# Performance work log

Measured on AMD Instinct MI355X. Metric: run time of the kernel, lower is better.

## Reference

```python
import jax, jax.numpy as jnp
import numpy as np

B, T, H = 64, 1024, 256

def _lstm_cell(x, h, c, Wih, Whh, bih, bhh):
    # torch gate order: i, f, g, o
    gates = x @ Wih.T + h @ Whh.T + bih + bhh  # [B, 4H]
    i, f, g, o = jnp.split(gates, 4, axis=-1)
    i = jax.nn.sigmoid(i)
    f = jax.nn.sigmoid(f)
    g = jnp.tanh(g)
    o = jax.nn.sigmoid(o)
    c_new = f * c + i * g
    h_new = o * jnp.tanh(c_new)
    return h_new, c_new


def setup_inputs() -> dict:
    key = jax.random.key(0)
    ks = jax.random.split(key, 11)
    s = 1.0 / np.sqrt(H)
    def u(k, shape):
        return jax.random.uniform(k, shape, jnp.float32, -s, s)
    return {
        "x": jax.random.normal(ks[0], (B, T, 1), jnp.float32),
        "enc_Wih": u(ks[1], (4 * H, 1)),
        "enc_Whh": u(ks[2], (4 * H, H)),
        "enc_bih": u(ks[3], (4 * H,)),
        "enc_bhh": u(ks[4], (4 * H,)),
        "dec_Wih": u(ks[5], (4 * H, 1)),
        "dec_Whh": u(ks[6], (4 * H, H)),
        "dec_bih": u(ks[7], (4 * H,)),
        "dec_bhh": u(ks[8], (4 * H,)),
        "lin_W": u(ks[9], (1, 2 * H)),
        "lin_b": u(ks[10], (1,)),
    }


def reference(x, enc_Wih, enc_Whh, enc_bih, enc_bhh,
              dec_Wih, dec_Whh, dec_bih, dec_bhh, lin_W, lin_b):
    b = x.shape[0]
    h = x.shape[2] * 0  # placeholder, not used
    hidden = enc_Whh.shape[1]

    x_t = jnp.transpose(x, (1, 0, 2))  # [T, B, 1]

    # ---- encoder: single-layer LSTM over time ----
    def enc_step(carry, xt):
        hh, cc = carry
        hh, cc = _lstm_cell(xt, hh, cc, enc_Wih, enc_Whh, enc_bih, enc_bhh)
        return (hh, cc), hh
    h0 = jnp.zeros((b, hidden), x.dtype)
    (h_last, _), enc_seq = jax.lax.scan(enc_step, (h0, h0), x_t)
    encoder_states = jnp.transpose(enc_seq, (1, 0, 2))  # [B, T, H]

    # ---- decoder: LSTMCell + dot attention + linear, per step ----
    def dec_step(carry, xt):
        hx, cx = carry
        hx, cx = _lstm_cell(xt, hx, cx, dec_Wih, dec_Whh, dec_bih, dec_bhh)
        scores = jnp.einsum('bth,bh->bt', encoder_states, hx)  # dot attention
        attn = jax.nn.softmax(scores, axis=1)
        ctx = jnp.einsum('bt,bth->bh', attn, encoder_states)
        updated = jnp.concatenate([ctx, hx], axis=1)  # [B, 2H]
        res = updated @ lin_W.T + lin_b  # [B, 1]
        return (hx, cx), res

    cx0 = jnp.zeros_like(h_last)
    _, outs = jax.lax.scan(dec_step, (h_last, cx0), x_t)  # [T, B, 1]
    return jnp.transpose(outs, (1, 0, 2))  # [B, T, 1]
```

## Files before the change

### kernel.cpp

```cpp
#include <hip/hip_runtime.h>
#include <math.h>

#define HD 256
#define GD 1024
#define TT 1024
#define BB 64
#define NT 512

__device__ __forceinline__ float sig_(float x)  { return 1.f / (1.f + __expf(-x)); }
__device__ __forceinline__ float tanh_(float x) { return 1.f - 2.f / (1.f + __expf(2.f * x)); }

__global__ __launch_bounds__(256) void prep_kernel(
    const float* __restrict__ eW, const float* __restrict__ eb1, const float* __restrict__ eb2,
    const float* __restrict__ dW, const float* __restrict__ db1, const float* __restrict__ db2,
    float* __restrict__ WTe, float* __restrict__ WTd,
    float* __restrict__ be, float* __restrict__ bd,
    unsigned long long* __restrict__ ex_all)
{
    int idx = blockIdx.x * 256 + threadIdx.x;
    if (idx < GD * HD) {
        int j = idx / HD, k = idx % HD;
        WTe[k * GD + j] = eW[idx];
        WTd[k * GD + j] = dW[idx];
    }
    if (idx < GD) {
        be[idx] = eb1[idx] + eb2[idx];
        bd[idx] = db1[idx] + db2[idx];
    }
    if (idx < 2 * BB * 2 * 256) ex_all[idx] = 0ULL;
}

__global__ __launch_bounds__(NT, 2) void lstm_scan_coop(
    const float* __restrict__ x,
    const float* __restrict__ Wih,
    const float* __restrict__ bias,
    const float* __restrict__ WT,
    const float* __restrict__ h_init,
    float* __restrict__ states,
    unsigned long long* __restrict__ ex)
{
    const int b   = blockIdx.x & 63;
    const int q   = blockIdx.x >> 6;
    const int tid = threadIdx.x;
    const int s   = tid & 3;
    const int jj  = tid >> 2;
    const int gate = jj >> 5;
    const int kk0  = (jj & 31) * 2;
    const int r0   = gate * 64 + kk0;
    const int jg0  = gate * 256 + q * 64 + kk0;

    __shared__ float h_rep[4][264];
    __shared__ float act_s[256];
    __shared__ float x_s[TT];

    float4 w0[16], w1[16];
    {
        const float* basek = WT + (size_t)(s * 64) * GD;
        #pragma unroll
        for (int i = 0; i < 16; ++i) {
            const float* p0 = basek + (size_t)(4 * i) * GD + jg0;
            w0[i] = make_float4(p0[0], p0[GD], p0[2 * GD], p0[3 * GD]);
            const float* p1 = p0 + 1;
            w1[i] = make_float4(p1[0], p1[GD], p1[2 * GD], p1[3 * GD]);
        }
    }
    const float wih0 = Wih[jg0], wih1 = Wih[jg0 + 1];
    const float bj0  = bias[jg0], bj1  = bias[jg0 + 1];

    for (int i = tid; i < TT; i += NT) x_s[i] = x[b * TT + i];
    if (tid < 256) {
        float hv = h_init ? h_init[((size_t)b * TT + (TT - 1)) * HD + tid] : 0.f;
        h_rep[tid >> 6][tid & 63] = hv;
    }
    float c = 0.f;
    __syncthreads();

    for (int t = 0; t < TT; ++t) {
        const float xt = x_s[t];
        float a0, a1;
        if (s == 0) { a0 = fmaf(xt, wih0, bj0); a1 = fmaf(xt, wih1, bj1); }
        else        { a0 = 0.f;                 a1 = 0.f; }
        const float4* h4 = (const float4*)(&h_rep[s][0]);
        #pragma unroll
        for (int i = 0; i < 16; ++i) {
            float4 hv = h4[i];
            a0 = fmaf(hv.x, w0[i].x, a0); a0 = fmaf(hv.y, w0[i].y, a0);
            a0 = fmaf(hv.z, w0[i].z, a0); a0 = fmaf(hv.w, w0[i].w, a0);
            a1 = fmaf(hv.x, w1[i].x, a1); a1 = fmaf(hv.y, w1[i].y, a1);
            a1 = fmaf(hv.z, w1[i].z, a1); a1 = fmaf(hv.w, w1[i].w, a1);
        }
        a0 += __shfl_xor(a0, 1); a0 += __shfl_xor(a0, 2);
        a1 += __shfl_xor(a1, 1); a1 += __shfl_xor(a1, 2);
        if (s == 0) {
            float2 av;
            av.x = (gate == 2) ? tanh_(a0) : sig_(a0);
            av.y = (gate == 2) ? tanh_(a1) : sig_(a1);
            *(float2*)(&act_s[r0]) = av;
        }
        __syncthreads();

        unsigned long long* slot = ex + ((size_t)b * 2 + (t & 1)) * 256;
        if (tid < 256) {
            const int dq = tid >> 6, dk = tid & 63;
            if (dq == q) {
                float gi = act_s[dk], gf = act_s[64 + dk], gg = act_s[128 + dk], go = act_s[192 + dk];
                c = fmaf(gf, c, gi * gg);
                float h = go * tanh_(c);
                h_rep[q][dk] = h;
                states[((size_t)(b * TT + t)) * HD + tid] = h;
                unsigned long long pk = ((unsigned long long)(unsigned)(t + 1) << 32)
                                      | (unsigned long long)__float_as_uint(h);
                __hip_atomic_store(&slot[tid], pk, __ATOMIC_RELAXED, __HIP_MEMORY_SCOPE_AGENT);
            } else {
                unsigned long long u;
                do {
                    u = __hip_atomic_load(&slot[tid], __ATOMIC_RELAXED, __HIP_MEMORY_SCOPE_AGENT);
                } while ((unsigned)(u >> 32) != (unsigned)(t + 1));
                h_rep[dq][dk] = __uint_as_float((unsigned)u);
            }
        }
        __syncthreads();
    }
}

__global__ __launch_bounds__(256) void proj_kernel(
    const float* __restrict__ enc_states, const float* __restrict__ dec_hs,
    const float* __restrict__ linW, float* __restrict__ ew, float* __restrict__ hw)
{
    const int lane = threadIdx.x & 63;
    const int wid  = blockIdx.x * 4 + (threadIdx.x >> 6);
    const int nw   = gridDim.x * 4;
    const float4 w1 = ((const float4*)linW)[lane];
    const float4 w2 = ((const float4*)(linW + HD))[lane];
    for (int o = wid; o < BB * TT; o += nw) {
        float4 v1 = ((const float4*)(enc_states + (size_t)o * HD))[lane];
        float4 v2 = ((const float4*)(dec_hs     + (size_t)o * HD))[lane];
        float s1 = v1.x * w1.x + v1.y * w1.y + v1.z * w1.z + v1.w * w1.w;
        float s2 = v2.x * w2.x + v2.y * w2.y + v2.z * w2.z + v2.w * w2.w;
        #pragma unroll
        for (int m = 1; m < 64; m <<= 1) {
            s1 += __shfl_xor(s1, m);
            s2 += __shfl_xor(s2, m);
        }
        if (lane == 0) { ew[o] = s1; hw[o] = s2; }
    }
}

#define TD  16
#define TEC 256
#define KC  32
__global__ __launch_bounds__(256) void attn_kernel(
    const float* __restrict__ enc_states,
    const float* __restrict__ dec_hs,
    const float* __restrict__ ew, const float* __restrict__ hw,
    const float* __restrict__ lin_b,
    float* __restrict__ out)
{
    const int b   = blockIdx.y;
    const int td0 = blockIdx.x * TD;
    const int tid = threadIdx.x;
    const int tdt = tid >> 5;
    const int tet = tid & 31;

    __shared__ float Hx[HD][TD + 1];
    __shared__ float E[KC][TEC];

    {
        const int td  = tid >> 4;
        const int k16 = (tid & 15) * 16;
        const float* src = dec_hs + ((size_t)b * TT + td0 + td) * HD + k16;
        #pragma unroll
        for (int qq = 0; qq < 4; ++qq) {
            float4 v = ((const float4*)(src + qq * 4))[0];
            Hx[k16 + qq * 4 + 0][td] = v.x;
            Hx[k16 + qq * 4 + 1][td] = v.y;
            Hx[k16 + qq * 4 + 2][td] = v.z;
            Hx[k16 + qq * 4 + 3][td] = v.w;
        }
    }

    float M[2]  = {-1e30f, -1e30f};
    float Nm[2] = {0.f, 0.f};
    float Dn[2] = {0.f, 0.f};

    for (int tc = 0; tc < TT / TEC; ++tc) {
        const int te0 = tc * TEC;
        float S[2][8] = {{0.f}};
        for (int kc = 0; kc < HD / KC; ++kc) {
            const int k0 = kc * KC;
            __syncthreads();
            {
                const float* src = enc_states + ((size_t)b * TT + te0 + tid) * HD + k0;
                #pragma unroll
                for (int qq = 0; qq < 8; ++qq) {
                    float4 v = ((const float4*)(src + qq * 4))[0];
                    E[qq * 4 + 0][tid] = v.x;
                    E[qq * 4 + 1][tid] = v.y;
                    E[qq * 4 + 2][tid] = v.z;
                    E[qq * 4 + 3][tid] = v.w;
                }
            }
            __syncthreads();
            #pragma unroll
            for (int k = 0; k < KC; ++k) {
                const float a0 = Hx[k0 + k][tdt * 2 + 0];
                const float a1 = Hx[k0 + k][tdt * 2 + 1];
                #pragma unroll
                for (int i = 0; i < 8; ++i) {
                    const float e = E[k][tet + 32 * i];
                    S[0][i] = fmaf(a0, e, S[0][i]);
                    S[1][i] = fmaf(a1, e, S[1][i]);
                }
            }
        }
        float ewv[8];
        #pragma unroll
        for (int i = 0; i < 8; ++i) ewv[i] = ew[(size_t)b * TT + te0 + tet + 32 * i];
        #pragma unroll
        for (int r = 0; r < 2; ++r) {
            float cm = S[r][0];
            #pragma unroll
            for (int i = 1; i < 8; ++i) cm = fmaxf(cm, S[r][i]);
            #pragma unroll
            for (int m = 1; m < 32; m <<= 1) cm = fmaxf(cm, __shfl_xor(cm, m));
            const float newM  = fmaxf(M[r], cm);
            const float scale = __expf(M[r] - newM);
            float nl = 0.f, dl = 0.f;
            #pragma unroll
            for (int i = 0; i < 8; ++i) {
                const float p = __expf(S[r][i] - newM);
                dl += p;
                nl = fmaf(p, ewv[i], nl);
            }
            #pragma unroll
            for (int m = 1; m < 32; m <<= 1) {
                nl += __shfl_xor(nl, m);
                dl += __shfl_xor(dl, m);
            }
            Nm[r] = Nm[r] * scale + nl;
            Dn[r] = Dn[r] * scale + dl;
            M[r]  = newM;
        }
    }

    if (tet == 0) {
        const float lb = lin_b[0];
        #pragma unroll
        for (int r = 0; r < 2; ++r) {
            const int td = td0 + tdt * 2 + r;
            out[(size_t)b * TT + td] = Nm[r] / Dn[r] + hw[(size_t)b * TT + td] + lb;
        }
    }
}

extern "C" void kernel_launch(void* const* d_in, const int* in_sizes, int n_in,
                              void* d_out, int out_size, void* d_ws, size_t ws_size,
                              hipStream_t stream)
{
    const float* x    = (const float*)d_in[0];
    const float* eWih = (const float*)d_in[1];
    const float* eWhh = (const float*)d_in[2];
    const float* ebih = (const float*)d_in[3];
    const float* ebhh = (const float*)d_in[4];
    const float* dWih = (const float*)d_in[5];
    const float* dWhh = (const float*)d_in[6];
    const float* dbih = (const float*)d_in[7];
    const float* dbhh = (const float*)d_in[8];
    const float* linW = (const float*)d_in[9];
    const float* linb = (const float*)d_in[10];
    float* out = (float*)d_out;

    float* p = (float*)d_ws;
    float* WTe = p;        p += (size_t)GD * HD;
    float* WTd = p;        p += (size_t)GD * HD;
    float* be  = p;        p += GD;
    float* bd  = p;        p += GD;
    float* enc_states = p; p += (size_t)BB * TT * HD;
    float* dec_hs = p;     p += (size_t)BB * TT * HD;
    float* ew = p;         p += (size_t)BB * TT;
    float* hw = p;         p += (size_t)BB * TT;
    unsigned long long* ex_e = (unsigned long long*)p; p += (size_t)BB * 2 * 256 * 2;
    unsigned long long* ex_d = (unsigned long long*)p; p += (size_t)BB * 2 * 256 * 2;

    prep_kernel<<<(GD * HD + 255) / 256, 256, 0, stream>>>(
        eWhh, ebih, ebhh, dWhh, dbih, dbhh, WTe, WTd, be, bd, ex_e);

    {
        const float* hi = nullptr;
        void* args[] = {(void*)&x, (void*)&eWih, (void*)&be, (void*)&WTe,
                        (void*)&hi, (void*)&enc_states, (void*)&ex_e};
        hipLaunchCooperativeKernel((void*)lstm_scan_coop, dim3(256), dim3(NT),
                                   args, 0, stream);
    }
    {
        const float* hi = enc_states;
        void* args[] = {(void*)&x, (void*)&dWih, (void*)&bd, (void*)&WTd,
                        (void*)&hi, (void*)&dec_hs, (void*)&ex_d};
        hipLaunchCooperativeKernel((void*)lstm_scan_coop, dim3(256), dim3(NT),
                                   args, 0, stream);
    }

    proj_kernel<<<256, 256, 0, stream>>>(enc_states, dec_hs, linW, ew, hw);
    attn_kernel<<<dim3(TT / TD, BB), 256, 0, stream>>>(enc_states, dec_hs, ew, hw, linb, out);
}
```

Baseline: 4.240 ms.

## Split LSTM dot accumulators, publish h earlier, and widen attention query tile

The recurrent gate dot product now uses two independent accumulator chains to shorten the FMA dependency chain. The atomic publish of h to other blocks is moved ahead of the local shared-memory and global stores, shortening the cross-block critical path. The attention kernel now processes 32 decoder steps per block (4 per thread via a float4 shared-memory read) instead of 16, doubling reuse of each loaded encoder tile and halving the grid. The trade-off is more registers per thread and fewer blocks.

```diff
diff --git a/kernel.cpp b/kernel.cpp
--- a/kernel.cpp
+++ b/kernel.cpp
@@ -77,18 +77,28 @@
 
     for (int t = 0; t < TT; ++t) {
         const float xt = x_s[t];
-        float a0, a1;
-        if (s == 0) { a0 = fmaf(xt, wih0, bj0); a1 = fmaf(xt, wih1, bj1); }
-        else        { a0 = 0.f;                 a1 = 0.f; }
+        float a0p, a1p, a0q = 0.f, a1q = 0.f;
+        if (s == 0) { a0p = fmaf(xt, wih0, bj0); a1p = fmaf(xt, wih1, bj1); }
+        else        { a0p = 0.f;                 a1p = 0.f; }
         const float4* h4 = (const float4*)(&h_rep[s][0]);
         #pragma unroll
-        for (int i = 0; i < 16; ++i) {
+        for (int i = 0; i < 8; ++i) {
             float4 hv = h4[i];
-            a0 = fmaf(hv.x, w0[i].x, a0); a0 = fmaf(hv.y, w0[i].y, a0);
-            a0 = fmaf(hv.z, w0[i].z, a0); a0 = fmaf(hv.w, w0[i].w, a0);
-            a1 = fmaf(hv.x, w1[i].x, a1); a1 = fmaf(hv.y, w1[i].y, a1);
-            a1 = fmaf(hv.z, w1[i].z, a1); a1 = fmaf(hv.w, w1[i].w, a1);
-        }
+            a0p = fmaf(hv.x, w0[i].x, a0p); a0p = fmaf(hv.y, w0[i].y, a0p);
+            a0p = fmaf(hv.z, w0[i].z, a0p); a0p = fmaf(hv.w, w0[i].w, a0p);
+            a1p = fmaf(hv.x, w1[i].x, a1p); a1p = fmaf(hv.y, w1[i].y, a1p);
+            a1p = fmaf(hv.z, w1[i].z, a1p); a1p = fmaf(hv.w, w1[i].w, a1p);
+        }
+        #pragma unroll
+        for (int i = 8; i < 16; ++i) {
+            float4 hv = h4[i];
+            a0q = fmaf(hv.x, w0[i].x, a0q); a0q = fmaf(hv.y, w0[i].y, a0q);
+            a0q = fmaf(hv.z, w0[i].z, a0q); a0q = fmaf(hv.w, w0[i].w, a0q);
+            a1q = fmaf(hv.x, w1[i].x, a1q); a1q = fmaf(hv.y, w1[i].y, a1q);
+            a1q = fmaf(hv.z, w1[i].z, a1q); a1q = fmaf(hv.w, w1[i].w, a1q);
+        }
+        float a0 = a0p + a0q;
+        float a1 = a1p + a1q;
         a0 += __shfl_xor(a0, 1); a0 += __shfl_xor(a0, 2);
         a1 += __shfl_xor(a1, 1); a1 += __shfl_xor(a1, 2);
         if (s == 0) {
@@ -106,11 +116,11 @@
                 float gi = act_s[dk], gf = act_s[64 + dk], gg = act_s[128 + dk], go = act_s[192 + dk];
                 c = fmaf(gf, c, gi * gg);
                 float h = go * tanh_(c);
-                h_rep[q][dk] = h;
-                states[((size_t)(b * TT + t)) * HD + tid] = h;
                 unsigned long long pk = ((unsigned long long)(unsigned)(t + 1) << 32)
                                       | (unsigned long long)__float_as_uint(h);
                 __hip_atomic_store(&slot[tid], pk, __ATOMIC_RELAXED, __HIP_MEMORY_SCOPE_AGENT);
+                h_rep[q][dk] = h;
+                states[((size_t)(b * TT + t)) * HD + tid] = h;
             } else {
                 unsigned long long u;
                 do {
@@ -146,9 +156,9 @@
     }
 }
 
-#define TD  16
-#define TEC 256
-#define KC  32
+#define TD2  32
+#define TEC2 256
+#define KC2  32
 __global__ __launch_bounds__(256) void attn_kernel(
     const float* __restrict__ enc_states,
     const float* __restrict__ dec_hs,
@@ -157,37 +167,37 @@
     float* __restrict__ out)
 {
     const int b   = blockIdx.y;
-    const int td0 = blockIdx.x * TD;
+    const int td0 = blockIdx.x * TD2;
     const int tid = threadIdx.x;
     const int tdt = tid >> 5;
     const int tet = tid & 31;
 
-    __shared__ float Hx[HD][TD + 1];
-    __shared__ float E[KC][TEC];
+    __shared__ float Hx[HD][TD2 + 4];
+    __shared__ float E[KC2][TEC2];
 
     {
-        const int td  = tid >> 4;
-        const int k16 = (tid & 15) * 16;
-        const float* src = dec_hs + ((size_t)b * TT + td0 + td) * HD + k16;
-        #pragma unroll
-        for (int qq = 0; qq < 4; ++qq) {
+        const int td = tid >> 3;
+        const int kc = (tid & 7) * 32;
+        const float* src = dec_hs + ((size_t)b * TT + td0 + td) * HD + kc;
+        #pragma unroll
+        for (int qq = 0; qq < 8; ++qq) {
             float4 v = ((const float4*)(src + qq * 4))[0];
-            Hx[k16 + qq * 4 + 0][td] = v.x;
-            Hx[k16 + qq * 4 + 1][td] = v.y;
-            Hx[k16 + qq * 4 + 2][td] = v.z;
-            Hx[k16 + qq * 4 + 3][td] = v.w;
-        }
-    }
-
-    float M[2]  = {-1e30f, -1e30f};
-    float Nm[2] = {0.f, 0.f};
-    float Dn[2] = {0.f, 0.f};
-
-    for (int tc = 0; tc < TT / TEC; ++tc) {
-        const int te0 = tc * TEC;
-        float S[2][8] = {{0.f}};
-        for (int kc = 0; kc < HD / KC; ++kc) {
-            const int k0 = kc * KC;
+            Hx[kc + qq * 4 + 0][td] = v.x;
+            Hx[kc + qq * 4 + 1][td] = v.y;
+            Hx[kc + qq * 4 + 2][td] = v.z;
+            Hx[kc + qq * 4 + 3][td] = v.w;
+        }
+    }
+
+    float M[4]  = {-1e30f, -1e30f, -1e30f, -1e30f};
+    float Nm[4] = {0.f, 0.f, 0.f, 0.f};
+    float Dn[4] = {0.f, 0.f, 0.f, 0.f};
+
+    for (int tc = 0; tc < TT / TEC2; ++tc) {
+        const int te0 = tc * TEC2;
+        float S[4][8] = {{0.f}};
+        for (int kc = 0; kc < HD / KC2; ++kc) {
+            const int k0 = kc * KC2;
             __syncthreads();
             {
                 const float* src = enc_states + ((size_t)b * TT + te0 + tid) * HD + k0;
@@ -201,15 +211,16 @@
                 }
             }
             __syncthreads();
-            #pragma unroll
-            for (int k = 0; k < KC; ++k) {
-                const float a0 = Hx[k0 + k][tdt * 2 + 0];
-                const float a1 = Hx[k0 + k][tdt * 2 + 1];
+            #pragma unroll 4
+            for (int k = 0; k < KC2; ++k) {
+                const float4 hx4 = *(const float4*)(&Hx[k0 + k][tdt * 4]);
                 #pragma unroll
                 for (int i = 0; i < 8; ++i) {
                     const float e = E[k][tet + 32 * i];
-                    S[0][i] = fmaf(a0, e, S[0][i]);
-                    S[1][i] = fmaf(a1, e, S[1][i]);
+                    S[0][i] = fmaf(hx4.x, e, S[0][i]);
+                    S[1][i] = fmaf(hx4.y, e, S[1][i]);
+                    S[2][i] = fmaf(hx4.z, e, S[2][i]);
+                    S[3][i] = fmaf(hx4.w, e, S[3][i]);
                 }
             }
         }
@@ -217,7 +228,7 @@
         #pragma unroll
         for (int i = 0; i < 8; ++i) ewv[i] = ew[(size_t)b * TT + te0 + tet + 32 * i];
         #pragma unroll
-        for (int r = 0; r < 2; ++r) {
+        for (int r = 0; r < 4; ++r) {
             float cm = S[r][0];
             #pragma unroll
             for (int i = 1; i < 8; ++i) cm = fmaxf(cm, S[r][i]);
@@ -246,8 +257,8 @@
     if (tet == 0) {
         const float lb = lin_b[0];
         #pragma unroll
-        for (int r = 0; r < 2; ++r) {
-            const int td = td0 + tdt * 2 + r;
+        for (int r = 0; r < 4; ++r) {
+            const int td = td0 + tdt * 4 + r;
             out[(size_t)b * TT + td] = Nm[r] / Dn[r] + hw[(size_t)b * TT + td] + lb;
         }
     }
@@ -301,5 +312,5 @@
     }
 
     proj_kernel<<<256, 256, 0, stream>>>(enc_states, dec_hs, linW, ew, hw);
-    attn_kernel<<<dim3(TT / TD, BB), 256, 0, stream>>>(enc_states, dec_hs, ew, hw, linb, out);
-}
+    attn_kernel<<<dim3(TT / TD2, BB), 256, 0, stream>>>(enc_states, dec_hs, ew, hw, linb, out);
+}
```

Result: faster. 3.864 ms (-8.9%).
